# Performance work log

Measured on AMD Instinct MI355X. Metric: run time of the kernel, lower is better.

The kernel has to match this reference:

```python
import jax, jax.numpy as jnp
import numpy as np
from jax import lax

B, QL, VL, D, H, K = 8, 512, 2048, 1024, 8, 10
DH = D // H  # per-head dim = 128


def setup_inputs() -> dict:
    key = jax.random.key(0)
    ks = jax.random.split(key, 12)
    s = 0.02
    return {
        "Q": jax.random.normal(ks[0], (B, QL, D), jnp.float32),
        "V": jax.random.normal(ks[1], (B, VL, D), jnp.float32),
        "last_align": jax.random.uniform(ks[2], (B, QL), jnp.float32),
        "conv_w": jax.random.normal(ks[3], (K, 1, 3), jnp.float32) * s,
        "conv_b": jnp.zeros((K,), jnp.float32),
        "Wq": jax.random.normal(ks[4], (D, D), jnp.float32) * s,
        "bq": jnp.zeros((D,), jnp.float32),
        "Wv": jax.random.normal(ks[5], (D, D), jnp.float32) * s,
        "bv": jnp.zeros((D,), jnp.float32),
        "Wu": jax.random.normal(ks[6], (D, K), jnp.float32) * s,
        "bu": jnp.zeros((D,), jnp.float32),
        "bias": jax.random.uniform(ks[7], (D,), jnp.float32, -0.1, 0.1),
        "fc_w": jax.random.normal(ks[8], (D, 2 * D), jnp.float32) * s,
        "fc_b": jnp.zeros((D,), jnp.float32),
    }


def reference(Q, V, last_align, conv_w, conv_b, Wq, bq, Wv, bv, Wu, bu, bias, fc_w, fc_b):
    b, qlen, d_model = Q.shape
    vlen = V.shape[1]
    # location feature: conv1d over last_align -> (B, K, qlen) -> (B, qlen, K)
    u = lax.conv_general_dilated(last_align[:, None, :], conv_w, (1,), [(1, 1)],
                                 dimension_numbers=("NCH", "OIH", "NCH"))
    U = jnp.transpose(u + conv_b[None, :, None], (0, 2, 1))  # (B, qlen, K)
    # fused projections + bias adds
    q_s = Q @ Wq.T + bq + U @ Wu.T + bu + bias  # (B, qlen, D)
    v_s = V @ Wv.T + bv                          # (B, vlen, D)
    q_s = q_s.reshape(b, qlen, H, DH)
    v_s = v_s.reshape(b, vlen, H, DH)
    score = jnp.einsum("bqhd,bvhd->bhqv", q_s, v_s) / np.sqrt(DH).astype(jnp.float32)
    # sigmoid smoothing normalization (not softmax)
    score = jax.nn.sigmoid(score)
    align = score / jnp.sum(score, axis=-1, keepdims=True)  # (B, H, qlen, vlen)
    context = jnp.einsum("bhqv,bvhd->bqhd", align, v_s).reshape(b, qlen, d_model)
    combined = jnp.concatenate([context, Q], axis=-1)  # (B, qlen, 2D)
    output = jnp.tanh(combined @ fc_w.T + fc_b)        # (B, qlen, D)
    # torch returns align flattened head-major: (H*B, qlen, vlen)
    align_t = jnp.transpose(align, (1, 0, 2, 3)).reshape(H * b, qlen, vlen)
    return output, align_t
```

## Files before the change

kernel.cpp:

```cpp
#include <hip/hip_runtime.h>

typedef __attribute__((ext_vector_type(8))) short short8;
typedef __attribute__((ext_vector_type(4))) short short4v;
typedef __attribute__((ext_vector_type(4))) float f32x4;

static __device__ __forceinline__ short f2bf(float x) {
    unsigned u = __builtin_bit_cast(unsigned, x);
    unsigned r = (u + 0x7fffu + ((u >> 16) & 1u)) >> 16;
    return (short)r;
}

static __device__ __forceinline__ void gld16(const short* g, short* l) {
    __builtin_amdgcn_global_load_lds((const __attribute__((address_space(1))) void*)g,
                                     (__attribute__((address_space(3))) void*)l, 16, 0, 0);
}

#define QL 512
#define VL 2048
#define DM 1024
#define NH 8
#define DH 128
#define NB 8
#define KQ 1088

__global__ void prep_k(const float* __restrict__ Q, const float* __restrict__ V,
                       const float* __restrict__ la, const float* __restrict__ cw,
                       const float* __restrict__ cb,
                       const float* __restrict__ Wq, const float* __restrict__ bq,
                       const float* __restrict__ Wv, const float* __restrict__ Wu,
                       const float* __restrict__ bu, const float* __restrict__ bias,
                       const float* __restrict__ fcw,
                       float* __restrict__ cbias, short* __restrict__ Aq,
                       short* __restrict__ comb, short* __restrict__ Vb,
                       short* __restrict__ Bq, short* __restrict__ Bv,
                       short* __restrict__ Bfc) {
    const int blk = blockIdx.x, tid = threadIdx.x;
    if (blk < 4) {
        int i = blk * 256 + tid;
        if (i < DM) cbias[i] = bq[i] + bu[i] + bias[i];
    } else if (blk < 20) {
        int m = (blk - 4) * 256 + tid;
        if (m >= NB * QL) return;
        int b = m >> 9, t = m & 511;
        const float* l = la + b * QL;
        float lm = (t > 0)      ? l[t - 1] : 0.f;
        float l0 = l[t];
        float lp = (t < QL - 1) ? l[t + 1] : 0.f;
        short* row = Aq + (size_t)m * KQ + 1024;
#pragma unroll
        for (int k = 0; k < 10; ++k)
            row[k] = f2bf(cb[k] + lm * cw[k * 3 + 0] + l0 * cw[k * 3 + 1] + lp * cw[k * 3 + 2]);
        for (int k = 10; k < 64; ++k) row[k] = 0;
    } else if (blk < 2068) {
        int id = (blk - 20) * 256 + tid;
        int m = id >> 7, kc = (id & 127) * 8;
        const float* p = Q + (size_t)m * DM + kc;
        float4 f0 = *(const float4*)p;
        float4 f1 = *(const float4*)(p + 4);
        short8 v;
        v[0]=f2bf(f0.x); v[1]=f2bf(f0.y); v[2]=f2bf(f0.z); v[3]=f2bf(f0.w);
        v[4]=f2bf(f1.x); v[5]=f2bf(f1.y); v[6]=f2bf(f1.z); v[7]=f2bf(f1.w);
        *(short8*)(Aq + (size_t)m * KQ + kc) = v;
        *(short8*)(comb + (size_t)m * (2 * DM) + DM + kc) = v;
    } else if (blk < 10260) {
        int id = (blk - 2068) * 256 + tid;
        const float* p = V + (size_t)id * 8;
        float4 f0 = *(const float4*)p;
        float4 f1 = *(const float4*)(p + 4);
        short8 v;
        v[0]=f2bf(f0.x); v[1]=f2bf(f0.y); v[2]=f2bf(f0.z); v[3]=f2bf(f0.w);
        v[4]=f2bf(f1.x); v[5]=f2bf(f1.y); v[6]=f2bf(f1.z); v[7]=f2bf(f1.w);
        *(short8*)(Vb + (size_t)id * 8) = v;
    } else {
        int id = (blk - 10260) * 256 + tid;
        const int nq = DM * KQ;
        const int nv = DM * DM;
        const int nf = DM * 2 * DM;
        if (id < nq) {
            int n = id / KQ, k = id % KQ;
            float v = (k < 1024) ? Wq[(size_t)n * 1024 + k]
                                 : ((k < 1034) ? Wu[n * 10 + (k - 1024)] : 0.f);
            Bq[id] = f2bf(v);
        } else if (id < nq + nv) {
            int j = id - nq;
            Bv[j] = f2bf(Wv[j]);
        } else if (id < nq + nv + nf) {
            int j = id - nq - nv;
            Bfc[j] = f2bf(fcw[j]);
        }
    }
}

template <int MODE>
__global__ __launch_bounds__(256) void gemm2_k(
    const short* __restrict__ A, const short* __restrict__ B,
    const float* __restrict__ bias, void* __restrict__ out0,
    short* __restrict__ outT, int M, int N, int K, int out_ld) {
    __shared__ short As[128 * 64];
    __shared__ short Bs[128 * 64];
    const int tid = threadIdx.x;
    const int lane = tid & 63, wave = tid >> 6;
    const int g = lane >> 4, c = lane & 15;
    const int nbm = M >> 7;
    const int x = blockIdx.x & 7, j = blockIdx.x >> 3;
    const int bm = x * (nbm >> 3) + (j >> 3);
    const int bn = j & 7;
    const int wr = wave >> 1, wc = wave & 1;

    const int srow = lane >> 3, scol = (lane & 7) * 8;
    const short* ag = A + (size_t)(bm * 128 + wave * 32 + srow) * K + scol;
    const short* bg = B + (size_t)(bn * 128 + wave * 32 + srow) * K + scol;

    f32x4 acc[4][4] = {};
    for (int k0 = 0; k0 < K; k0 += 64) {
#pragma unroll
        for (int ch = 0; ch < 4; ++ch) {
            gld16(ag + (size_t)(ch * 8) * K + k0, As + (wave * 32 + ch * 8) * 64);
            gld16(bg + (size_t)(ch * 8) * K + k0, Bs + (wave * 32 + ch * 8) * 64);
        }
        __syncthreads();
#pragma unroll
        for (int ks = 0; ks < 2; ++ks) {
            short8 af[4], bfr[4];
#pragma unroll
            for (int mi = 0; mi < 4; ++mi) af[mi] = *(const short8*)(As + (wr * 64 + mi * 16 + c) * 64 + ks * 32 + g * 8);
#pragma unroll
            for (int ni = 0; ni < 4; ++ni) bfr[ni] = *(const short8*)(Bs + (wc * 64 + ni * 16 + c) * 64 + ks * 32 + g * 8);
#pragma unroll
            for (int mi = 0; mi < 4; ++mi)
#pragma unroll
                for (int ni = 0; ni < 4; ++ni)
                    acc[mi][ni] = __builtin_amdgcn_mfma_f32_16x16x32_bf16(af[mi], bfr[ni], acc[mi][ni], 0, 0, 0);
        }
        __syncthreads();
    }

    const int m0 = bm * 128 + wr * 64, n0 = bn * 128 + wc * 64;
#pragma unroll
    for (int ni = 0; ni < 4; ++ni) {
        int n = n0 + ni * 16 + c;
        float bn_ = bias[n];
#pragma unroll
        for (int mi = 0; mi < 4; ++mi) {
            int mb = m0 + mi * 16 + 4 * g;
            f32x4 v = acc[mi][ni];
            if constexpr (MODE == 2) {
                float* o = (float*)out0;
#pragma unroll
                for (int r = 0; r < 4; ++r)
                    o[(size_t)(mb + r) * out_ld + n] = tanhf(v[r] + bn_);
            } else {
                short* o = (short*)out0;
                short4v pk;
#pragma unroll
                for (int r = 0; r < 4; ++r) {
                    pk[r] = f2bf(v[r] + bn_);
                    o[(size_t)(mb + r) * out_ld + n] = pk[r];
                }
                if constexpr (MODE == 0) {
                    int h = n >> 7, hd = n & 127;
                    int bb = mb >> 11, vv = mb & 2047;
                    *(short4v*)(outT + ((size_t)((bb * NH + h) * DH + hd)) * VL + vv) = pk;
                }
            }
        }
    }
}

__global__ __launch_bounds__(256) void rowsum_k(
    const short* __restrict__ qs, const short* __restrict__ vs,
    float* __restrict__ rsum_part) {
    __shared__ short As[128 * 64];
    __shared__ short Bs[128 * 64];
    const int blk = blockIdx.x;
    const int xr = blk & 7, t = blk >> 3;
    const int bn = t & 15;
    const int bm = (t >> 4) & 3;
    const int bh = ((t >> 6) << 3) | xr;
    const int h = bh & 7, b = bh >> 3;

    const int tid = threadIdx.x;
    const int lane = tid & 63, wave = tid >> 6;
    const int g = lane >> 4, c = lane & 15;
    const int wr = wave >> 1, wc = wave & 1;
    const float sc = 0.08838834764831845f;

    const int srow = lane >> 3, scol = (lane & 7) * 8;
    const short* ag = qs + (size_t)(b * QL + bm * 128 + wave * 32 + srow) * DM + h * DH + scol;
    const short* bg = vs + (size_t)(b * VL + bn * 128 + wave * 32 + srow) * DM + h * DH + scol;

    f32x4 acc[4][4] = {};
    for (int k0 = 0; k0 < DH; k0 += 64) {
#pragma unroll
        for (int ch = 0; ch < 4; ++ch) {
            gld16(ag + (size_t)(ch * 8) * DM + k0, As + (wave * 32 + ch * 8) * 64);
            gld16(bg + (size_t)(ch * 8) * DM + k0, Bs + (wave * 32 + ch * 8) * 64);
        }
        __syncthreads();
#pragma unroll
        for (int ks = 0; ks < 2; ++ks) {
            short8 af[4], bfr[4];
#pragma unroll
            for (int mi = 0; mi < 4; ++mi) af[mi] = *(const short8*)(As + (wr * 64 + mi * 16 + c) * 64 + ks * 32 + g * 8);
#pragma unroll
            for (int ni = 0; ni < 4; ++ni) bfr[ni] = *(const short8*)(Bs + (wc * 64 + ni * 16 + c) * 64 + ks * 32 + g * 8);
#pragma unroll
            for (int mi = 0; mi < 4; ++mi)
#pragma unroll
                for (int ni = 0; ni < 4; ++ni)
                    acc[mi][ni] = __builtin_amdgcn_mfma_f32_16x16x32_bf16(af[mi], bfr[ni], acc[mi][ni], 0, 0, 0);
        }
        __syncthreads();
    }

    float psum[4][4];
#pragma unroll
    for (int mi = 0; mi < 4; ++mi)
#pragma unroll
        for (int r = 0; r < 4; ++r) psum[mi][r] = 0.f;

    const int m0 = bm * 128 + wr * 64;
#pragma unroll
    for (int ni = 0; ni < 4; ++ni) {
#pragma unroll
        for (int mi = 0; mi < 4; ++mi) {
            f32x4 v = acc[mi][ni];
#pragma unroll
            for (int r = 0; r < 4; ++r)
                psum[mi][r] += __builtin_amdgcn_rcpf(1.f + __expf(-v[r] * sc));
        }
    }
#pragma unroll
    for (int off = 1; off < 16; off <<= 1)
#pragma unroll
        for (int mi = 0; mi < 4; ++mi)
#pragma unroll
            for (int r = 0; r < 4; ++r) psum[mi][r] += __shfl_xor(psum[mi][r], off);
    if (c == 0) {
#pragma unroll
        for (int mi = 0; mi < 4; ++mi)
#pragma unroll
            for (int r = 0; r < 4; ++r) {
                int q = m0 + mi * 16 + 4 * g + r;
                rsum_part[(size_t)(bh * QL + q) * 32 + bn * 2 + wc] = psum[mi][r];
            }
    }
}

__global__ __launch_bounds__(256, 3) void fat2_k(
    const short* __restrict__ qs, const short* __restrict__ vs,
    const short* __restrict__ vsT, const float* __restrict__ rsum_part,
    float* __restrict__ align_out, float* __restrict__ ctxp) {
    __shared__ short Vs[64][136];
    __shared__ short Vt[128][72];
    __shared__ short Pl[4][16][72];
    __shared__ float rsl[64];

    const int blk = blockIdx.x;
    const int xr = blk & 7, t = blk >> 3;
    const int vh = t & 1;
    const int qt = (t >> 1) & 7;
    const int bh = ((t >> 4) << 3) | xr;
    const int h = bh & 7, b = bh >> 3;
    const int q0 = qt * 64;
    const int vbeg = vh * 1024;

    const int tid = threadIdx.x, wave = tid >> 6, lane = tid & 63;
    const int g = lane >> 4, c = lane & 15;
    const float sc = 0.08838834764831845f;

    if (tid < 64) {
        const float* p = rsum_part + (size_t)(bh * QL + q0 + tid) * 32;
        float s = 0.f;
#pragma unroll
        for (int jj = 0; jj < 32; ++jj) s += p[jj];
        rsl[tid] = __builtin_amdgcn_rcpf(s);
    }
    __syncthreads();

    float invr[4];
#pragma unroll
    for (int r = 0; r < 4; ++r) invr[r] = rsl[wave * 16 + 4 * g + r];

    short8 qa[4];
    const short* qb = qs + ((size_t)(b * QL + q0 + wave * 16 + c)) * DM + h * DH + g * 8;
#pragma unroll
    for (int ks = 0; ks < 4; ++ks) qa[ks] = *(const short8*)(qb + ks * 32);

    const int vsrow = tid >> 2, vscq = (tid & 3) * 32;
    const short* vsg = vs + ((size_t)(b * VL + vsrow)) * DM + h * DH + vscq;
    const int vtrow = tid >> 1, vtcq = (tid & 1) * 32;
    const short* vtg = vsT + ((size_t)(bh * DH + vtrow)) * VL + vtcq;

    float* ao = align_out + ((size_t)((h * NB + b) * QL + q0 + wave * 16)) * VL;

    short8 pv_s[4], pv_t[4];
#pragma unroll
    for (int i = 0; i < 4; ++i) pv_s[i] = *(const short8*)(vsg + (size_t)vbeg * DM + i * 8);
#pragma unroll
    for (int i = 0; i < 4; ++i) pv_t[i] = *(const short8*)(vtg + vbeg + i * 8);

    f32x4 ctx[8] = {};
    for (int tc = 0; tc < 16; ++tc) {
        const int v0 = vbeg + tc * 64;
#pragma unroll
        for (int i = 0; i < 4; ++i) *(short8*)&Vs[vsrow][vscq + i * 8] = pv_s[i];
#pragma unroll
        for (int i = 0; i < 4; ++i) *(short8*)&Vt[vtrow][vtcq + i * 8] = pv_t[i];
        __syncthreads();
        if (tc + 1 < 16) {
            const int v1 = v0 + 64;
#pragma unroll
            for (int i = 0; i < 4; ++i) pv_s[i] = *(const short8*)(vsg + (size_t)v1 * DM + i * 8);
#pragma unroll
            for (int i = 0; i < 4; ++i) pv_t[i] = *(const short8*)(vtg + v1 + i * 8);
        }

#pragma unroll
        for (int ni = 0; ni < 4; ++ni) {
            f32x4 s = {0.f, 0.f, 0.f, 0.f};
#pragma unroll
            for (int ks = 0; ks < 4; ++ks)
                s = __builtin_amdgcn_mfma_f32_16x16x32_bf16(qa[ks], *(const short8*)&Vs[ni * 16 + c][ks * 32 + g * 8], s, 0, 0, 0);
#pragma unroll
            for (int r = 0; r < 4; ++r) {
                float pn = __builtin_amdgcn_rcpf(1.f + __expf(-s[r] * sc)) * invr[r];
                __builtin_nontemporal_store(pn, &ao[(size_t)(4 * g + r) * VL + v0 + ni * 16 + c]);
                Pl[wave][4 * g + r][ni * 16 + c] = f2bf(pn);
            }
        }
        short8 pa0 = *(const short8*)&Pl[wave][c][g * 8];
        short8 pa1 = *(const short8*)&Pl[wave][c][32 + g * 8];
#pragma unroll
        for (int df = 0; df < 8; ++df) {
            ctx[df] = __builtin_amdgcn_mfma_f32_16x16x32_bf16(pa0, *(const short8*)&Vt[df * 16 + c][g * 8], ctx[df], 0, 0, 0);
            ctx[df] = __builtin_amdgcn_mfma_f32_16x16x32_bf16(pa1, *(const short8*)&Vt[df * 16 + c][32 + g * 8], ctx[df], 0, 0, 0);
        }
        __syncthreads();
    }

    float* cp = ctxp + ((size_t)((bh * 8 + qt) * 2 + vh)) * (64 * 128);
#pragma unroll
    for (int df = 0; df < 8; ++df)
#pragma unroll
        for (int r = 0; r < 4; ++r)
            cp[(size_t)(wave * 16 + 4 * g + r) * 128 + df * 16 + c] = ctx[df][r];
}

__global__ void ctxred_k(const float* __restrict__ ctxp, short* __restrict__ comb) {
    int id = blockIdx.x * 256 + threadIdx.x;
    int d0 = (id & 15) * 8;
    int r  = (id >> 4) & 63;
    int qt = (id >> 10) & 7;
    int bh = id >> 13;
    int h = bh & 7, b = bh >> 3;
    const float* p0 = ctxp + ((size_t)((bh * 8 + qt) * 2)) * 8192 + r * 128 + d0;
    const float* p1 = p0 + 8192;
    short8 o;
#pragma unroll
    for (int jj = 0; jj < 8; ++jj) o[jj] = f2bf(p0[jj] + p1[jj]);
    *(short8*)(comb + ((size_t)(b * QL + qt * 64 + r)) * (2 * DM) + h * DH + d0) = o;
}

extern "C" void kernel_launch(void* const* d_in, const int* in_sizes, int n_in,
                              void* d_out, int out_size, void* d_ws, size_t ws_size,
                              hipStream_t stream) {
    (void)in_sizes; (void)n_in; (void)out_size; (void)ws_size;
    const float* Q    = (const float*)d_in[0];
    const float* V    = (const float*)d_in[1];
    const float* la   = (const float*)d_in[2];
    const float* cw   = (const float*)d_in[3];
    const float* cb   = (const float*)d_in[4];
    const float* Wq   = (const float*)d_in[5];
    const float* bq   = (const float*)d_in[6];
    const float* Wv   = (const float*)d_in[7];
    const float* bv   = (const float*)d_in[8];
    const float* Wu   = (const float*)d_in[9];
    const float* bu   = (const float*)d_in[10];
    const float* bias = (const float*)d_in[11];
    const float* fcw  = (const float*)d_in[12];
    const float* fcb  = (const float*)d_in[13];

    float* out = (float*)d_out;
    float* align_out = out + (size_t)NB * QL * DM;

    char* w = (char*)d_ws;
    short* Vb   = (short*)w; w += (size_t)16384 * 1024 * 2;
    short* Aq   = (short*)w; w += (size_t)4096 * KQ * 2;
    short* comb = (short*)w; w += (size_t)4096 * 2048 * 2;
    short* Bq   = (short*)w; w += (size_t)1024 * KQ * 2;
    short* Bvw  = (short*)w; w += (size_t)1024 * 1024 * 2;
    short* Bfc  = (short*)w; w += (size_t)1024 * 2048 * 2;
    short* vsb  = (short*)w; w += (size_t)16384 * 1024 * 2;
    short* vsT  = (short*)w; w += (size_t)16384 * 1024 * 2;
    short* qsb  = (short*)w; w += (size_t)4096 * 1024 * 2;
    float* rsum_part = (float*)w; w += (size_t)32768 * 32 * 4;
    float* ctxp = (float*)w; w += (size_t)1024 * 64 * 128 * 4;
    float* cbias = (float*)w; w += 1024 * 4;

    prep_k<<<26900, 256, 0, stream>>>(Q, V, la, cw, cb, Wq, bq, Wv, Wu, bu, bias, fcw,
                                      cbias, Aq, comb, Vb, Bq, Bvw, Bfc);
    gemm2_k<0><<<1024, 256, 0, stream>>>(Vb, Bvw, bv, vsb, vsT, 16384, 1024, 1024, 1024);
    gemm2_k<1><<<256, 256, 0, stream>>>(Aq, Bq, cbias, qsb, nullptr, 4096, 1024, KQ, 1024);
    rowsum_k<<<4096, 256, 0, stream>>>(qsb, vsb, rsum_part);
    fat2_k<<<1024, 256, 0, stream>>>(qsb, vsb, vsT, rsum_part, align_out, ctxp);
    ctxred_k<<<2048, 256, 0, stream>>>(ctxp, comb);
    gemm2_k<2><<<256, 256, 0, stream>>>(comb, Bfc, fcb, out, nullptr, 4096, 1024, 2048, 1024);
}
```

Before: 311.4 us.

## Merge V/Q projection launches, store bf16 context partials, adjust LDS padding and priorities

The V and Q projection GEMMs now run as one 1280-block launch through a shared device body, which removes a launch and lets the tail of one GEMM overlap the other. The per-half context partials are written as bf16 instead of fp32, halving the traffic into the reduction kernel at the cost of an extra rounding step before the sum. LDS row padding in fat2_k changes (136→132, 72→70), and s_setprio is raised around the MFMA blocks to favour matrix issue over the exp and store work. The new padding may alter bank-conflict behaviour and 16-byte alignment of the vector LDS reads.

```diff
diff --git a/kernel.cpp b/kernel.cpp
--- a/kernel.cpp
+++ b/kernel.cpp
@@ -92,19 +92,14 @@
 }
 
 template <int MODE>
-__global__ __launch_bounds__(256) void gemm2_k(
+static __device__ __forceinline__ void gemm_body(
+    short* As, short* Bs,
     const short* __restrict__ A, const short* __restrict__ B,
     const float* __restrict__ bias, void* __restrict__ out0,
-    short* __restrict__ outT, int M, int N, int K, int out_ld) {
-    __shared__ short As[128 * 64];
-    __shared__ short Bs[128 * 64];
+    short* __restrict__ outT, int K, int out_ld, int bm, int bn) {
     const int tid = threadIdx.x;
     const int lane = tid & 63, wave = tid >> 6;
     const int g = lane >> 4, c = lane & 15;
-    const int nbm = M >> 7;
-    const int x = blockIdx.x & 7, j = blockIdx.x >> 3;
-    const int bm = x * (nbm >> 3) + (j >> 3);
-    const int bn = j & 7;
     const int wr = wave >> 1, wc = wave & 1;
 
     const int srow = lane >> 3, scol = (lane & 7) * 8;
@@ -165,6 +160,33 @@
             }
         }
     }
+}
+
+__global__ __launch_bounds__(256) void gemmvq_k(
+    const short* __restrict__ Vb, const short* __restrict__ Bvw,
+    const float* __restrict__ bv, short* __restrict__ vsb, short* __restrict__ vsT,
+    const short* __restrict__ Aq, const short* __restrict__ Bq,
+    const float* __restrict__ cbias, short* __restrict__ qsb) {
+    __shared__ short As[128 * 64];
+    __shared__ short Bs[128 * 64];
+    const int blk = blockIdx.x;
+    if (blk < 1024) {
+        const int x = blk & 7, j = blk >> 3;
+        gemm_body<0>(As, Bs, Vb, Bvw, bv, vsb, vsT, 1024, 1024, x * 16 + (j >> 3), j & 7);
+    } else {
+        const int b2 = blk - 1024;
+        const int x = b2 & 7, j = b2 >> 3;
+        gemm_body<1>(As, Bs, Aq, Bq, cbias, qsb, nullptr, KQ, 1024, x * 4 + (j >> 3), j & 7);
+    }
+}
+
+__global__ __launch_bounds__(256) void gemmfc_k(
+    const short* __restrict__ comb, const short* __restrict__ Bfc,
+    const float* __restrict__ fcb, float* __restrict__ out) {
+    __shared__ short As[128 * 64];
+    __shared__ short Bs[128 * 64];
+    const int x = blockIdx.x & 7, j = blockIdx.x >> 3;
+    gemm_body<2>(As, Bs, comb, Bfc, fcb, out, nullptr, 2048, 1024, x * 4 + (j >> 3), j & 7);
 }
 
 __global__ __launch_bounds__(256) void rowsum_k(
@@ -250,10 +272,10 @@
 __global__ __launch_bounds__(256, 3) void fat2_k(
     const short* __restrict__ qs, const short* __restrict__ vs,
     const short* __restrict__ vsT, const float* __restrict__ rsum_part,
-    float* __restrict__ align_out, float* __restrict__ ctxp) {
-    __shared__ short Vs[64][136];
-    __shared__ short Vt[128][72];
-    __shared__ short Pl[4][16][72];
+    float* __restrict__ align_out, short* __restrict__ ctxp) {
+    __shared__ short Vs[64][132];
+    __shared__ short Vt[128][70];
+    __shared__ short Pl[4][16][70];
     __shared__ float rsl[64];
 
     const int blk = blockIdx.x;
@@ -319,9 +341,11 @@
 #pragma unroll
         for (int ni = 0; ni < 4; ++ni) {
             f32x4 s = {0.f, 0.f, 0.f, 0.f};
+            __builtin_amdgcn_s_setprio(1);
 #pragma unroll
             for (int ks = 0; ks < 4; ++ks)
                 s = __builtin_amdgcn_mfma_f32_16x16x32_bf16(qa[ks], *(const short8*)&Vs[ni * 16 + c][ks * 32 + g * 8], s, 0, 0, 0);
+            __builtin_amdgcn_s_setprio(0);
 #pragma unroll
             for (int r = 0; r < 4; ++r) {
                 float pn = __builtin_amdgcn_rcpf(1.f + __expf(-s[r] * sc)) * invr[r];
@@ -331,34 +355,42 @@
         }
         short8 pa0 = *(const short8*)&Pl[wave][c][g * 8];
         short8 pa1 = *(const short8*)&Pl[wave][c][32 + g * 8];
+        __builtin_amdgcn_s_setprio(1);
 #pragma unroll
         for (int df = 0; df < 8; ++df) {
             ctx[df] = __builtin_amdgcn_mfma_f32_16x16x32_bf16(pa0, *(const short8*)&Vt[df * 16 + c][g * 8], ctx[df], 0, 0, 0);
             ctx[df] = __builtin_amdgcn_mfma_f32_16x16x32_bf16(pa1, *(const short8*)&Vt[df * 16 + c][32 + g * 8], ctx[df], 0, 0, 0);
         }
-        __syncthreads();
-    }
-
-    float* cp = ctxp + ((size_t)((bh * 8 + qt) * 2 + vh)) * (64 * 128);
+        __builtin_amdgcn_s_setprio(0);
+        __syncthreads();
+    }
+
+    short* cp = ctxp + ((size_t)((bh * 8 + qt) * 2 + vh)) * (64 * 128);
 #pragma unroll
     for (int df = 0; df < 8; ++df)
 #pragma unroll
         for (int r = 0; r < 4; ++r)
-            cp[(size_t)(wave * 16 + 4 * g + r) * 128 + df * 16 + c] = ctx[df][r];
-}
-
-__global__ void ctxred_k(const float* __restrict__ ctxp, short* __restrict__ comb) {
+            cp[(size_t)(wave * 16 + 4 * g + r) * 128 + df * 16 + c] = f2bf(ctx[df][r]);
+}
+
+__global__ void ctxred_k(const short* __restrict__ ctxp, short* __restrict__ comb) {
     int id = blockIdx.x * 256 + threadIdx.x;
     int d0 = (id & 15) * 8;
     int r  = (id >> 4) & 63;
     int qt = (id >> 10) & 7;
     int bh = id >> 13;
     int h = bh & 7, b = bh >> 3;
-    const float* p0 = ctxp + ((size_t)((bh * 8 + qt) * 2)) * 8192 + r * 128 + d0;
-    const float* p1 = p0 + 8192;
+    const short* p0 = ctxp + ((size_t)((bh * 8 + qt) * 2)) * 8192 + r * 128 + d0;
+    const short* p1 = p0 + 8192;
+    short8 a = *(const short8*)p0;
+    short8 bb = *(const short8*)p1;
     short8 o;
 #pragma unroll
-    for (int jj = 0; jj < 8; ++jj) o[jj] = f2bf(p0[jj] + p1[jj]);
+    for (int jj = 0; jj < 8; ++jj) {
+        float fa = __builtin_bit_cast(float, ((unsigned)(unsigned short)a[jj]) << 16);
+        float fb = __builtin_bit_cast(float, ((unsigned)(unsigned short)bb[jj]) << 16);
+        o[jj] = f2bf(fa + fb);
+    }
     *(short8*)(comb + ((size_t)(b * QL + qt * 64 + r)) * (2 * DM) + h * DH + d0) = o;
 }
 
@@ -395,15 +427,14 @@
     short* vsT  = (short*)w; w += (size_t)16384 * 1024 * 2;
     short* qsb  = (short*)w; w += (size_t)4096 * 1024 * 2;
     float* rsum_part = (float*)w; w += (size_t)32768 * 32 * 4;
-    float* ctxp = (float*)w; w += (size_t)1024 * 64 * 128 * 4;
+    short* ctxp = (short*)w; w += (size_t)1024 * 64 * 128 * 2;
     float* cbias = (float*)w; w += 1024 * 4;
 
     prep_k<<<26900, 256, 0, stream>>>(Q, V, la, cw, cb, Wq, bq, Wv, Wu, bu, bias, fcw,
                                       cbias, Aq, comb, Vb, Bq, Bvw, Bfc);
-    gemm2_k<0><<<1024, 256, 0, stream>>>(Vb, Bvw, bv, vsb, vsT, 16384, 1024, 1024, 1024);
-    gemm2_k<1><<<256, 256, 0, stream>>>(Aq, Bq, cbias, qsb, nullptr, 4096, 1024, KQ, 1024);
+    gemmvq_k<<<1280, 256, 0, stream>>>(Vb, Bvw, bv, vsb, vsT, Aq, Bq, cbias, qsb);
     rowsum_k<<<4096, 256, 0, stream>>>(qsb, vsb, rsum_part);
     fat2_k<<<1024, 256, 0, stream>>>(qsb, vsb, vsT, rsum_part, align_out, ctxp);
     ctxred_k<<<2048, 256, 0, stream>>>(ctxp, comb);
-    gemm2_k<2><<<256, 256, 0, stream>>>(comb, Bfc, fcb, out, nullptr, 4096, 1024, 2048, 1024);
-}
+    gemmfc_k<<<256, 256, 0, stream>>>(comb, Bfc, fcb, out);
+}
```

New measurement: 317.8 us. 1.02x slower.
